# Kernel tuning notes

Measured on AMD Instinct MI355X. Metric: run time of the kernel, lower is better.

The kernel has to match this reference:

```python
import jax, jax.numpy as jnp
import numpy as np

N = 100000
E = 1600000
IN_C = 128
OUT_C = 64
ALPHA = 0.2  # LeakyReLU negative slope


def _xavier(key, shape, gain=1.414):
    fan_in, fan_out = shape[-2] if len(shape) > 1 else shape[-1], shape[-1]
    bound = gain * np.sqrt(6.0 / (shape[0] * 0 + (shape[-2] if len(shape) > 1 else 1) + shape[-1])) if False else gain * np.sqrt(6.0 / (sum(shape)))
    return jax.random.uniform(key, shape, jnp.float32, -bound, bound)


def setup_inputs() -> dict:
    key = jax.random.key(0)
    k_x, k_s, k_o, k_w, k_a = jax.random.split(key, 5)
    x = jax.random.normal(k_x, (N, IN_C), jnp.float32)
    # edge list with no self-loops (so remove_self_loops is a no-op)
    src = jax.random.randint(k_s, (E,), 0, N)
    off = jax.random.randint(k_o, (E,), 1, N)
    dst = (src + off) % N
    edge_index = jnp.stack([src, dst]).astype(jnp.int64)
    W = _xavier(k_w, (IN_C, OUT_C))
    a = _xavier(k_a, (1, 2 * OUT_C))
    return {"x": x, "W": W, "a": a, "edge_index": edge_index}


def reference(x, W, a, edge_index):
    h = x @ W                               # [N, D]
    n, d = h.shape
    loops = jnp.arange(n, dtype=edge_index.dtype)
    src = jnp.concatenate([edge_index[0], loops])   # add_self_loops
    dst = jnp.concatenate([edge_index[1], loops])
    # (cat(h[src], h[dst]) * a).sum(-1) == h[src]@a1 + h[dst]@a2
    a1, a2 = a[0, :d], a[0, d:]
    s = h @ a1                              # [N]
    t = h @ a2                              # [N]
    edge_e = jnp.exp(jax.nn.leaky_relu(s[src] + t[dst], negative_slope=ALPHA))  # [E+N]
    e_expsum = jax.ops.segment_sum(edge_e, src, num_segments=n)                  # [N]
    h_prime = jax.ops.segment_sum(edge_e[:, None] * h[dst], src, num_segments=n)  # [N, D]
    return h_prime / e_expsum[:, None]
```

## Files before the change

### kernel.cpp

```cpp
#include <hip/hip_runtime.h>
#include <math.h>

#define IN_C 128
#define OUT_C 64
#define ALPHA 0.2f

#define LDK 136

#define BSH 7
#define NPB 128
#define MAXB 1024
#define PA_EPT 4
#define PA_THREADS 1024
#define PA_TILE (PA_THREADS * PA_EPT)
#define CHUNK 4096

typedef __attribute__((ext_vector_type(8))) short short8;
typedef __attribute__((ext_vector_type(4))) float v4f;

__device__ __forceinline__ ushort f2b(float f) {
  unsigned u = __float_as_uint(f);
  u += 0x7fffu + ((u >> 16) & 1u);
  return (ushort)(u >> 16);
}

__global__ __launch_bounds__(256) void gemm_st_kernel(
    const float* __restrict__ x, const float* __restrict__ W,
    const float* __restrict__ a, ushort* __restrict__ hb,
    float* __restrict__ s, float* __restrict__ t, int* __restrict__ gcur,
    int nbuck, int cape, int n_nodes, int n_tiles) {
  __shared__ ushort xs[64 * LDK];
  __shared__ ushort ws[64 * LDK];

  const int tid = threadIdx.x;
  const int wave = tid >> 6;
  const int lane = tid & 63;
  const int li = lane & 15;
  const int quad = lane >> 4;

  if (blockIdx.x == 0) {
    for (int i = tid; i < nbuck; i += 256) gcur[i] = i * cape;
  }

  for (int i = tid; i < IN_C * OUT_C; i += 256) {
    const int k = i >> 6;
    const int n = i & 63;
    ws[n * LDK + k] = f2b(W[i]);
  }
  __syncthreads();

  short8 bfrag[4][4];
#pragma unroll
  for (int ct = 0; ct < 4; ++ct)
#pragma unroll
    for (int kk = 0; kk < 4; ++kk)
      bfrag[ct][kk] =
          *(const short8*)&ws[(ct * 16 + li) * LDK + kk * 32 + quad * 8];

  float a1v[4], a2v[4];
#pragma unroll
  for (int ct = 0; ct < 4; ++ct) {
    a1v[ct] = a[ct * 16 + li];
    a2v[ct] = a[OUT_C + ct * 16 + li];
  }

  for (int tile = blockIdx.x; tile < n_tiles; tile += gridDim.x) {
    const int row0 = tile * 64;

    __syncthreads();
    for (int i = tid; i < 64 * (IN_C / 4); i += 256) {
      const int r = i >> 5;
      const int c4 = i & 31;
      int row = row0 + r;
      row = row < n_nodes ? row : n_nodes - 1;
      const float4 v = *(const float4*)&x[(size_t)row * IN_C + c4 * 4];
      uint2 p;
      p.x = (unsigned)f2b(v.x) | ((unsigned)f2b(v.y) << 16);
      p.y = (unsigned)f2b(v.z) | ((unsigned)f2b(v.w) << 16);
      *(uint2*)&xs[r * LDK + c4 * 4] = p;
    }
    __syncthreads();

    v4f acc[4];
#pragma unroll
    for (int ct = 0; ct < 4; ++ct) acc[ct] = (v4f){0.f, 0.f, 0.f, 0.f};

    const int rbase = wave * 16;
#pragma unroll
    for (int kk = 0; kk < 4; ++kk) {
      const short8 af =
          *(const short8*)&xs[(rbase + li) * LDK + kk * 32 + quad * 8];
#pragma unroll
      for (int ct = 0; ct < 4; ++ct)
        acc[ct] = __builtin_amdgcn_mfma_f32_16x16x32_bf16(af, bfrag[ct][kk],
                                                          acc[ct], 0, 0, 0);
    }

    const int growbase = row0 + rbase + quad * 4;
    float ps[4] = {0.f, 0.f, 0.f, 0.f};
    float pt[4] = {0.f, 0.f, 0.f, 0.f};
#pragma unroll
    for (int ct = 0; ct < 4; ++ct) {
#pragma unroll
      for (int r = 0; r < 4; ++r) {
        const float hv = acc[ct][r];
        ps[r] += hv * a1v[ct];
        pt[r] += hv * a2v[ct];
        const int grow = growbase + r;
        if (grow < n_nodes)
          hb[(size_t)grow * OUT_C + ct * 16 + li] = f2b(hv);
      }
    }
#pragma unroll
    for (int m = 1; m <= 8; m <<= 1) {
#pragma unroll
      for (int r = 0; r < 4; ++r) {
        ps[r] += __shfl_xor(ps[r], m, 64);
        pt[r] += __shfl_xor(pt[r], m, 64);
      }
    }
    if (li < 4) {
      const int grow = growbase + li;
      if (grow < n_nodes) {
        const float sv = li == 0 ? ps[0] : li == 1 ? ps[1] : li == 2 ? ps[2] : ps[3];
        const float tv = li == 0 ? pt[0] : li == 1 ? pt[1] : li == 2 ? pt[2] : pt[3];
        s[grow] = sv;
        t[grow] = tv;
      }
    }
  }
}

__global__ __launch_bounds__(PA_THREADS) void pa_bin(
    const int* __restrict__ src, const int* __restrict__ dst,
    const float* __restrict__ s, const float* __restrict__ t,
    int* __restrict__ gcur, int2* __restrict__ pairs, int nbuck, int cape,
    int E) {
  __shared__ int hist[MAXB];
  __shared__ int cur[MAXB];
  const int tid = threadIdx.x;
  for (int i = tid; i < nbuck; i += PA_THREADS) hist[i] = 0;
  __syncthreads();

  const int e0 = blockIdx.x * PA_TILE + tid * PA_EPT;
  if (e0 + PA_EPT <= E) {
    const int4 v = *(const int4*)(src + e0);
    atomicAdd(&hist[v.x >> BSH], 1);
    atomicAdd(&hist[v.y >> BSH], 1);
    atomicAdd(&hist[v.z >> BSH], 1);
    atomicAdd(&hist[v.w >> BSH], 1);
  } else {
    for (int e = e0; e < E; ++e) atomicAdd(&hist[src[e] >> BSH], 1);
  }
  __syncthreads();

  for (int i = tid; i < nbuck; i += PA_THREADS) {
    const int c = hist[i];
    cur[i] = c ? atomicAdd(&gcur[i], c) : 0;
  }
  __syncthreads();

#define EMIT(sv, dv)                                                       \
  {                                                                        \
    const int bkt = (sv) >> BSH;                                           \
    const float z = s[sv] + t[dv];                                         \
    const float w = expf(z > 0.f ? z : ALPHA * z);                         \
    const int pos = atomicAdd(&cur[bkt], 1);                               \
    if (pos < (bkt + 1) * cape)                                            \
      pairs[pos] =                                                         \
          make_int2((((sv) & (NPB - 1)) << 25) | (dv), __float_as_int(w)); \
  }

  if (e0 + PA_EPT <= E) {
    const int4 sv = *(const int4*)(src + e0);
    const int4 dv = *(const int4*)(dst + e0);
    EMIT(sv.x, dv.x);
    EMIT(sv.y, dv.y);
    EMIT(sv.z, dv.z);
    EMIT(sv.w, dv.w);
  } else {
    for (int e = e0; e < E; ++e) {
      const int sv = src[e];
      const int dv = dst[e];
      EMIT(sv, dv);
    }
  }
#undef EMIT
}

#define ACC8(o, p, wgt)                                      \
  acc[(o) + 0] += (wgt)*__uint_as_float((p).x << 16);        \
  acc[(o) + 1] += (wgt)*__uint_as_float((p).x & 0xffff0000u);\
  acc[(o) + 2] += (wgt)*__uint_as_float((p).y << 16);        \
  acc[(o) + 3] += (wgt)*__uint_as_float((p).y & 0xffff0000u);\
  acc[(o) + 4] += (wgt)*__uint_as_float((p).z << 16);        \
  acc[(o) + 5] += (wgt)*__uint_as_float((p).z & 0xffff0000u);\
  acc[(o) + 6] += (wgt)*__uint_as_float((p).w << 16);        \
  acc[(o) + 7] += (wgt)*__uint_as_float((p).w & 0xffff0000u);

__global__ __launch_bounds__(256) void aggregate_sorted(
    const int2* __restrict__ pairs, const int* __restrict__ gcur,
    const uint4* __restrict__ hb4, const float* __restrict__ s,
    const float* __restrict__ t, float* __restrict__ out, int n_nodes,
    int cape) {
  __shared__ int2 sl[CHUNK];
  __shared__ int cnt[NPB];
  __shared__ int loffs[NPB];
  __shared__ int cur[NPB];
  __shared__ int w0tot_sh;

  const int b = blockIdx.x;
  const int tid = threadIdx.x;
  const int base = b * cape;
  int fill = gcur[b] - base;
  fill = fill < cape ? fill : cape;

  const int local = tid >> 1;
  const int half = tid & 1;

  float acc[32];
#pragma unroll
  for (int i = 0; i < 32; ++i) acc[i] = 0.f;
  float den = 0.f;

  for (int c0 = 0; c0 < fill; c0 += CHUNK) {
    const int clen = min(CHUNK, fill - c0);
    if (tid < NPB) cnt[tid] = 0;
    __syncthreads();

    int2 pw[CHUNK / 256];
#pragma unroll
    for (int j = 0; j < CHUNK / 256; ++j) {
      const int k = j * 256 + tid;
      if (k < clen) {
        pw[j] = pairs[base + c0 + k];
        atomicAdd(&cnt[((unsigned)pw[j].x) >> 25], 1);
      }
    }
    __syncthreads();

    int c = 0, incl = 0;
    if (tid < NPB) {
      c = cnt[tid];
      incl = c;
#pragma unroll
      for (int off = 1; off < 64; off <<= 1) {
        const int o = __shfl_up(incl, off, 64);
        if ((tid & 63) >= off) incl += o;
      }
      if (tid == 63) w0tot_sh = incl;
    }
    __syncthreads();
    if (tid < NPB) {
      if (tid >= 64) incl += w0tot_sh;
      loffs[tid] = incl - c;
      cur[tid] = incl - c;
    }
    __syncthreads();

#pragma unroll
    for (int j = 0; j < CHUNK / 256; ++j) {
      const int k = j * 256 + tid;
      if (k < clen) {
        const int lo = ((unsigned)pw[j].x) >> 25;
        const int pos = atomicAdd(&cur[lo], 1);
        sl[pos] = make_int2(pw[j].x & 0x1ffffff, pw[j].y);
      }
    }
    __syncthreads();

    const int s0 = loffs[local];
    const int s1 = s0 + cnt[local];
    int e = s0;
    for (; e + 3 < s1; e += 4) {
      const int2 ea = sl[e];
      const int2 eb = sl[e + 1];
      const int2 ec = sl[e + 2];
      const int2 ed = sl[e + 3];
      const uint4* ra = &hb4[(size_t)ea.x * 8 + half * 4];
      const uint4* rb = &hb4[(size_t)eb.x * 8 + half * 4];
      const uint4* rc = &hb4[(size_t)ec.x * 8 + half * 4];
      const uint4* rd = &hb4[(size_t)ed.x * 8 + half * 4];
      const uint4 pa0 = ra[0], pa1 = ra[1], pa2 = ra[2], pa3 = ra[3];
      const uint4 pb0 = rb[0], pb1 = rb[1], pb2 = rb[2], pb3 = rb[3];
      const uint4 pc0 = rc[0], pc1 = rc[1], pc2 = rc[2], pc3 = rc[3];
      const uint4 pd0 = rd[0], pd1 = rd[1], pd2 = rd[2], pd3 = rd[3];
      const float wa = __int_as_float(ea.y);
      const float wb = __int_as_float(eb.y);
      const float wc = __int_as_float(ec.y);
      const float wd = __int_as_float(ed.y);
      ACC8(0, pa0, wa) ACC8(8, pa1, wa) ACC8(16, pa2, wa) ACC8(24, pa3, wa)
      ACC8(0, pb0, wb) ACC8(8, pb1, wb) ACC8(16, pb2, wb) ACC8(24, pb3, wb)
      ACC8(0, pc0, wc) ACC8(8, pc1, wc) ACC8(16, pc2, wc) ACC8(24, pc3, wc)
      ACC8(0, pd0, wd) ACC8(8, pd1, wd) ACC8(16, pd2, wd) ACC8(24, pd3, wd)
      den += (wa + wb) + (wc + wd);
    }
    for (; e < s1; ++e) {
      const int2 ea = sl[e];
      const uint4* ra = &hb4[(size_t)ea.x * 8 + half * 4];
      const uint4 pa0 = ra[0], pa1 = ra[1], pa2 = ra[2], pa3 = ra[3];
      const float wa = __int_as_float(ea.y);
      ACC8(0, pa0, wa) ACC8(8, pa1, wa) ACC8(16, pa2, wa) ACC8(24, pa3, wa)
      den += wa;
    }
    __syncthreads();
  }

  const int u = b * NPB + local;
  if (u < n_nodes) {
    const float z0 = s[u] + t[u];
    const float w0 = expf(z0 > 0.f ? z0 : ALPHA * z0);
    const uint4* rs = &hb4[(size_t)u * 8 + half * 4];
    const uint4 q0 = rs[0], q1 = rs[1], q2 = rs[2], q3 = rs[3];
    ACC8(0, q0, w0) ACC8(8, q1, w0) ACC8(16, q2, w0) ACC8(24, q3, w0)
    den += w0;
    const float inv = 1.f / den;
#pragma unroll
    for (int q = 0; q < 8; ++q) {
      float4 o;
      o.x = acc[q * 4 + 0] * inv;
      o.y = acc[q * 4 + 1] * inv;
      o.z = acc[q * 4 + 2] * inv;
      o.w = acc[q * 4 + 3] * inv;
      *(float4*)&out[(size_t)u * OUT_C + half * 32 + q * 4] = o;
    }
  }
}

extern "C" void kernel_launch(void* const* d_in, const int* in_sizes, int n_in,
                              void* d_out, int out_size, void* d_ws,
                              size_t ws_size, hipStream_t stream) {
  const float* x = (const float*)d_in[0];
  const float* W = (const float*)d_in[1];
  const float* a = (const float*)d_in[2];
  const int* edge_index = (const int*)d_in[3];

  const int n_nodes = in_sizes[0] / IN_C;
  const int E = in_sizes[3] / 2;
  const int* src = edge_index;
  const int* dst = edge_index + E;

  float* out = (float*)d_out;

  const int nbuck = (n_nodes + NPB - 1) >> BSH;
  const int cape = (((E + nbuck - 1) / nbuck) + 768 + 15) & ~15;
  const int nblk_bin = (E + PA_TILE - 1) / PA_TILE;

  ushort* hb = (ushort*)d_ws;
  float* s = (float*)(hb + (size_t)n_nodes * OUT_C);
  float* t = s + n_nodes;
  int* gcur = (int*)(t + n_nodes);
  int2* pairs = (int2*)(gcur + MAXB);

  {
    const int n_tiles = (n_nodes + 63) / 64;
    const int ngrid = n_tiles < 512 ? n_tiles : 512;
    gemm_st_kernel<<<ngrid, 256, 0, stream>>>(x, W, a, hb, s, t, gcur, nbuck,
                                              cape, n_nodes, n_tiles);
  }

  pa_bin<<<nblk_bin, PA_THREADS, 0, stream>>>(src, dst, s, t, gcur, pairs,
                                              nbuck, cape, E);

  aggregate_sorted<<<nbuck, 256, 0, stream>>>(pairs, gcur, (const uint4*)hb, s,
                                              t, out, n_nodes, cape);
}
```

Before: 202.7 us.

## Defer edge weight computation to aggregation, shrinking binned pairs to 4 bytes

The binning kernel no longer gathers s/t or computes exp weights; it writes only the packed (local src, dst) index, halving the pairs buffer and the LDS staging array. The aggregation kernel now loads s[u] once per node, gathers t[dst] per edge and computes the LeakyReLU+exp weight there using the fast __expf. It also cuts the inner-loop unroll from 4 to 2 edges. The per-edge gather of t moves to the aggregation inner loop, where it sits alongside the hb row gathers, and less unrolling may reduce memory-level parallelism.

```diff
diff --git a/kernel.cpp b/kernel.cpp
--- a/kernel.cpp
+++ b/kernel.cpp
@@ -133,8 +133,7 @@
 
 __global__ __launch_bounds__(PA_THREADS) void pa_bin(
     const int* __restrict__ src, const int* __restrict__ dst,
-    const float* __restrict__ s, const float* __restrict__ t,
-    int* __restrict__ gcur, int2* __restrict__ pairs, int nbuck, int cape,
+    int* __restrict__ gcur, int* __restrict__ pairs, int nbuck, int cape,
     int E) {
   __shared__ int hist[MAXB];
   __shared__ int cur[MAXB];
@@ -160,15 +159,12 @@
   }
   __syncthreads();
 
-#define EMIT(sv, dv)                                                       \
-  {                                                                        \
-    const int bkt = (sv) >> BSH;                                           \
-    const float z = s[sv] + t[dv];                                         \
-    const float w = expf(z > 0.f ? z : ALPHA * z);                         \
-    const int pos = atomicAdd(&cur[bkt], 1);                               \
-    if (pos < (bkt + 1) * cape)                                            \
-      pairs[pos] =                                                         \
-          make_int2((((sv) & (NPB - 1)) << 25) | (dv), __float_as_int(w)); \
+#define EMIT(sv, dv)                                          \
+  {                                                           \
+    const int bkt = (sv) >> BSH;                              \
+    const int pos = atomicAdd(&cur[bkt], 1);                  \
+    if (pos < (bkt + 1) * cape)                               \
+      pairs[pos] = (((sv) & (NPB - 1)) << 25) | (dv);         \
   }
 
   if (e0 + PA_EPT <= E) {
@@ -199,11 +195,11 @@
   acc[(o) + 7] += (wgt)*__uint_as_float((p).w & 0xffff0000u);
 
 __global__ __launch_bounds__(256) void aggregate_sorted(
-    const int2* __restrict__ pairs, const int* __restrict__ gcur,
+    const int* __restrict__ pairs, const int* __restrict__ gcur,
     const uint4* __restrict__ hb4, const float* __restrict__ s,
     const float* __restrict__ t, float* __restrict__ out, int n_nodes,
     int cape) {
-  __shared__ int2 sl[CHUNK];
+  __shared__ int sl[CHUNK];
   __shared__ int cnt[NPB];
   __shared__ int loffs[NPB];
   __shared__ int cur[NPB];
@@ -217,6 +213,9 @@
 
   const int local = tid >> 1;
   const int half = tid & 1;
+  const int u = b * NPB + local;
+  const bool valid = u < n_nodes;
+  const float su = valid ? s[u] : 0.f;
 
   float acc[32];
 #pragma unroll
@@ -228,13 +227,13 @@
     if (tid < NPB) cnt[tid] = 0;
     __syncthreads();
 
-    int2 pw[CHUNK / 256];
+    int pw[CHUNK / 256];
 #pragma unroll
     for (int j = 0; j < CHUNK / 256; ++j) {
       const int k = j * 256 + tid;
       if (k < clen) {
         pw[j] = pairs[base + c0 + k];
-        atomicAdd(&cnt[((unsigned)pw[j].x) >> 25], 1);
+        atomicAdd(&cnt[((unsigned)pw[j]) >> 25], 1);
       }
     }
     __syncthreads();
@@ -262,9 +261,9 @@
     for (int j = 0; j < CHUNK / 256; ++j) {
       const int k = j * 256 + tid;
       if (k < clen) {
-        const int lo = ((unsigned)pw[j].x) >> 25;
+        const int lo = ((unsigned)pw[j]) >> 25;
         const int pos = atomicAdd(&cur[lo], 1);
-        sl[pos] = make_int2(pw[j].x & 0x1ffffff, pw[j].y);
+        sl[pos] = pw[j] & 0x1ffffff;
       }
     }
     __syncthreads();
@@ -272,44 +271,43 @@
     const int s0 = loffs[local];
     const int s1 = s0 + cnt[local];
     int e = s0;
-    for (; e + 3 < s1; e += 4) {
-      const int2 ea = sl[e];
-      const int2 eb = sl[e + 1];
-      const int2 ec = sl[e + 2];
-      const int2 ed = sl[e + 3];
-      const uint4* ra = &hb4[(size_t)ea.x * 8 + half * 4];
-      const uint4* rb = &hb4[(size_t)eb.x * 8 + half * 4];
-      const uint4* rc = &hb4[(size_t)ec.x * 8 + half * 4];
-      const uint4* rd = &hb4[(size_t)ed.x * 8 + half * 4];
+    for (; e + 1 < s1; e += 2) {
+      const int va = sl[e];
+      const int vb = sl[e + 1];
+      const float ta = t[va];
+      const float tb = t[vb];
+      const uint4* ra = &hb4[(size_t)va * 8 + half * 4];
+      const uint4* rb = &hb4[(size_t)vb * 8 + half * 4];
       const uint4 pa0 = ra[0], pa1 = ra[1], pa2 = ra[2], pa3 = ra[3];
       const uint4 pb0 = rb[0], pb1 = rb[1], pb2 = rb[2], pb3 = rb[3];
-      const uint4 pc0 = rc[0], pc1 = rc[1], pc2 = rc[2], pc3 = rc[3];
-      const uint4 pd0 = rd[0], pd1 = rd[1], pd2 = rd[2], pd3 = rd[3];
-      const float wa = __int_as_float(ea.y);
-      const float wb = __int_as_float(eb.y);
-      const float wc = __int_as_float(ec.y);
-      const float wd = __int_as_float(ed.y);
+      float za = su + ta;
+      float zb = su + tb;
+      za = za > 0.f ? za : ALPHA * za;
+      zb = zb > 0.f ? zb : ALPHA * zb;
+      const float wa = __expf(za);
+      const float wb = __expf(zb);
       ACC8(0, pa0, wa) ACC8(8, pa1, wa) ACC8(16, pa2, wa) ACC8(24, pa3, wa)
       ACC8(0, pb0, wb) ACC8(8, pb1, wb) ACC8(16, pb2, wb) ACC8(24, pb3, wb)
-      ACC8(0, pc0, wc) ACC8(8, pc1, wc) ACC8(16, pc2, wc) ACC8(24, pc3, wc)
-      ACC8(0, pd0, wd) ACC8(8, pd1, wd) ACC8(16, pd2, wd) ACC8(24, pd3, wd)
-      den += (wa + wb) + (wc + wd);
-    }
-    for (; e < s1; ++e) {
-      const int2 ea = sl[e];
-      const uint4* ra = &hb4[(size_t)ea.x * 8 + half * 4];
+      den += wa + wb;
+    }
+    if (e < s1) {
+      const int va = sl[e];
+      const float ta = t[va];
+      const uint4* ra = &hb4[(size_t)va * 8 + half * 4];
       const uint4 pa0 = ra[0], pa1 = ra[1], pa2 = ra[2], pa3 = ra[3];
-      const float wa = __int_as_float(ea.y);
+      float za = su + ta;
+      za = za > 0.f ? za : ALPHA * za;
+      const float wa = __expf(za);
       ACC8(0, pa0, wa) ACC8(8, pa1, wa) ACC8(16, pa2, wa) ACC8(24, pa3, wa)
       den += wa;
     }
     __syncthreads();
   }
 
-  const int u = b * NPB + local;
-  if (u < n_nodes) {
-    const float z0 = s[u] + t[u];
-    const float w0 = expf(z0 > 0.f ? z0 : ALPHA * z0);
+  if (valid) {
+    float z0 = su + t[u];
+    z0 = z0 > 0.f ? z0 : ALPHA * z0;
+    const float w0 = __expf(z0);
     const uint4* rs = &hb4[(size_t)u * 8 + half * 4];
     const uint4 q0 = rs[0], q1 = rs[1], q2 = rs[2], q3 = rs[3];
     ACC8(0, q0, w0) ACC8(8, q1, w0) ACC8(16, q2, w0) ACC8(24, q3, w0)
@@ -350,7 +348,7 @@
   float* s = (float*)(hb + (size_t)n_nodes * OUT_C);
   float* t = s + n_nodes;
   int* gcur = (int*)(t + n_nodes);
-  int2* pairs = (int2*)(gcur + MAXB);
+  int* pairs = gcur + MAXB;
 
   {
     const int n_tiles = (n_nodes + 63) / 64;
@@ -359,8 +357,8 @@
                                               cape, n_nodes, n_tiles);
   }
 
-  pa_bin<<<nblk_bin, PA_THREADS, 0, stream>>>(src, dst, s, t, gcur, pairs,
-                                              nbuck, cape, E);
+  pa_bin<<<nblk_bin, PA_THREADS, 0, stream>>>(src, dst, gcur, pairs, nbuck,
+                                              cape, E);
 
   aggregate_sorted<<<nbuck, 256, 0, stream>>>(pairs, gcur, (const uint4*)hb, s,
                                               t, out, n_nodes, cape);
```

Result: faster. 188.0 us (-7.3%).
